# Kernel tuning notes

Measured on AMD Instinct MI355X. Metric: run time of the kernel, lower is better.

## Reference

```python
import jax, jax.numpy as jnp
import numpy as np

CLASSES = 21
IOU_THRESH = 0.5
ALPHA, GAMMA = 0.25, 2.0
CLS_W, REG_W = 1.0, 1.0


def _make_boxes(key, shape):
    # valid xyxy boxes: x1<x2, y1<y2 inside unit square
    k1, k2 = jax.random.split(key)
    xy1 = jax.random.uniform(k1, shape[:-1] + (2,)) * 0.8
    wh = jax.random.uniform(k2, shape[:-1] + (2,)) * 0.19 + 0.01
    return jnp.concatenate([xy1, xy1 + wh], axis=-1).astype(jnp.float32)


def setup_inputs() -> dict:
    key = jax.random.key(0)
    k1, k2, k3, k4, k5 = jax.random.split(key, 5)
    B, A, T = 4, 49152, 50
    return {
        "classification_preds": jax.random.normal(k1, (B, A, CLASSES), dtype=jnp.float32),
        "boxes_preds": _make_boxes(k2, (B, A, 4)),
        "anchors": _make_boxes(k3, (B, A, 4)),
        "target_boxes": _make_boxes(k4, (B, T, 4)),
        "target_labels": jax.random.randint(k5, (B, T), 1, CLASSES),  # 1..20 (0=background)
    }


def compute_iou(a, b):
    # a: [T,4] xyxy, b: [A,4] xyxy -> [T,A]
    lt = jnp.maximum(a[:, None, :2], b[None, :, :2])
    rb = jnp.minimum(a[:, None, 2:], b[None, :, 2:])
    wh = jnp.clip(rb - lt, 0.0)
    inter = wh[..., 0] * wh[..., 1]
    area_a = (a[:, 2] - a[:, 0]) * (a[:, 3] - a[:, 1])
    area_b = (b[:, 2] - b[:, 0]) * (b[:, 3] - b[:, 1])
    union = area_a[:, None] + area_b[None, :] - inter
    return inter / jnp.clip(union, 1e-8)


def encode(boxes, anchors):
    # xyxy -> center offsets relative to anchors
    bc = (boxes[:, :2] + boxes[:, 2:]) * 0.5
    bwh = boxes[:, 2:] - boxes[:, :2]
    ac = (anchors[:, :2] + anchors[:, 2:]) * 0.5
    awh = anchors[:, 2:] - anchors[:, :2]
    txy = (bc - ac) / awh
    twh = jnp.log(bwh / awh)
    return jnp.concatenate([txy, twh], axis=-1)


def focal_loss(logits, targets):
    p = jax.nn.sigmoid(logits)
    ce = -(targets * jax.nn.log_sigmoid(logits) + (1.0 - targets) * jax.nn.log_sigmoid(-logits))
    pt = targets * p + (1.0 - targets) * (1.0 - p)
    alpha_t = targets * ALPHA + (1.0 - targets) * (1.0 - ALPHA)
    return alpha_t * (1.0 - pt) ** GAMMA * ce


def smooth_l1(x, y):
    d = jnp.abs(x - y)
    return jnp.where(d < 1.0, 0.5 * d * d, d - 0.5)


def reference(classification_preds, boxes_preds, anchors, target_boxes, target_labels):
    cls = classification_preds.reshape(-1, CLASSES)   # [A, C]
    box = boxes_preds.reshape(-1, 4)                  # [A, 4]
    anc = anchors.reshape(-1, 4)                      # [A, 4]
    tb = target_boxes.reshape(-1, 4)                  # [T, 4]
    tl = target_labels.reshape(-1)                    # [T]

    iou = compute_iou(tb, anc)                        # [T, A]
    max_iou = jnp.max(iou, axis=0)                    # [A]
    tid = jnp.argmax(iou, axis=0)                     # [A]
    pos = max_iou >= IOU_THRESH                       # [A]
    pos_cnt = jnp.sum(pos.astype(jnp.int32))
    norm = jnp.clip(pos_cnt, 1).astype(cls.dtype)

    onehot = jax.nn.one_hot(tl[tid], CLASSES, dtype=cls.dtype)        # [A, C]
    background = jax.nn.one_hot(0, CLASSES, dtype=cls.dtype)          # [C]
    cls_tgt = jnp.where(pos[:, None], onehot, background[None, :])    # [A, C]

    cls_loss = jnp.sum(focal_loss(cls, cls_tgt)) / norm

    enc_pred = encode(box, anc)                       # [A, 4]
    enc_tgt = encode(tb[tid], anc)                    # [A, 4]
    reg_elem = smooth_l1(enc_pred, enc_tgt) * pos[:, None].astype(cls.dtype)
    reg_loss = jnp.sum(reg_elem) / (norm * 4.0)       # mean over positive elements
    reg_loss = jnp.where(pos_cnt > 0, reg_loss, 0.0)

    wc = cls_loss * CLS_W
    wr = reg_loss * REG_W
    return (wc + wr, wc, wr)
```

## Files before the change

kernel.cpp:

```cpp
#include <hip/hip_runtime.h>


#define CLASSES 21
#define TPB 256
#define G 4

__global__ void prep_kernel(const float4* __restrict__ tb,
                            float* __restrict__ tarea, int T) {
    int t = blockIdx.x * blockDim.x + threadIdx.x;
    if (t < T) {
        float4 v = tb[t];
        tarea[t] = (v.z - v.x) * (v.w - v.y);
    }
}

__global__ __launch_bounds__(TPB)
void iou_kernel(const float4* __restrict__ anc,
                const float4* __restrict__ tbox,
                const float* __restrict__ tarea,
                float* __restrict__ pbI, float* __restrict__ pbU,
                int* __restrict__ pbT,
                int A, int T, int chunk) {
    int c  = blockIdx.x & (G - 1);
    int ab = blockIdx.x >> 2;
    int a  = ab * TPB + threadIdx.x;
    if (a >= A) return;

    float4 av = anc[a];
    float areaA = (av.z - av.x) * (av.w - av.y);

    int t0 = c * chunk;
    int t1 = min(T, t0 + chunk);
    float bI = 0.0f, bU = 1.0f;
    int bT = t0;
    #pragma unroll 10
    for (int t = t0; t < t1; ++t) {
        float4 tv = tbox[t];
        float ta = tarea[t];
        float lx = fmaxf(tv.x, av.x);
        float ly = fmaxf(tv.y, av.y);
        float rx = fminf(tv.z, av.z);
        float ry = fminf(tv.w, av.w);
        float w = fmaxf(rx - lx, 0.0f);
        float h = fmaxf(ry - ly, 0.0f);
        float inter = w * h;
        float uni = (ta + areaA) - inter;
        bool gt = inter * bU > bI * uni;
        bI = gt ? inter : bI;
        bU = gt ? uni : bU;
        bT = gt ? t : bT;
    }
    size_t o = (size_t)c * A + a;
    pbI[o] = bI;
    pbU[o] = bU;
    pbT[o] = bT;
}

__global__ __launch_bounds__(TPB)
void loss_kernel(const float* __restrict__ cls,
                 const float4* __restrict__ box,
                 const float4* __restrict__ anc,
                 const int* __restrict__ labels,
                 const float4* __restrict__ tbox,
                 const float* __restrict__ pbI, const float* __restrict__ pbU,
                 const int* __restrict__ pbT,
                 float* __restrict__ pc, float* __restrict__ pr,
                 float* __restrict__ pp,
                 int A) {
    __shared__ float s_cls[TPB * CLASSES];
    int tid = threadIdx.x;
    int a = blockIdx.x * TPB + tid;

    {
        const float4* g4 = (const float4*)(cls + (size_t)blockIdx.x * TPB * CLASSES);
        float4* s4 = (float4*)s_cls;
        int n4 = (TPB * CLASSES) / 4;
        int lim4 = min(n4, (int)(((size_t)A * CLASSES - (size_t)blockIdx.x * TPB * CLASSES) / 4));
        for (int i = tid; i < lim4; i += TPB) s4[i] = g4[i];
    }
    __syncthreads();

    float cls_p = 0.0f, reg_p = 0.0f, pos_p = 0.0f;

    if (a < A) {
        float bI = 0.0f, bU = 1.0f;
        int bT = 0;
        #pragma unroll
        for (int c = 0; c < G; ++c) {
            size_t o = (size_t)c * A + a;
            float oI = pbI[o];
            float oU = pbU[o];
            int   oT = pbT[o];
            if (c == 0) { bI = oI; bU = oU; bT = oT; }
            else {
                bool gt = oI * bU > bI * oU;
                bI = gt ? oI : bI;
                bU = gt ? oU : bU;
                bT = gt ? oT : bT;
            }
        }
        bool pos = (bI + bI) >= bU;

        int hot = pos ? labels[bT] : 0;
        const float* crow = s_cls + tid * CLASSES;
        float csum = 0.0f;
        #pragma unroll
        for (int j = 0; j < CLASSES; ++j) {
            float x = crow[j];
            float y = (j == hot) ? -x : x;
            float em = __expf(-fabsf(y));
            float sp = fmaxf(y, 0.0f) + __logf(1.0f + em);
            float r1 = __builtin_amdgcn_rcpf(1.0f + em);
            float sg = (y >= 0.0f) ? r1 : em * r1;
            float f = sg * sg * sp;
            csum = fmaf(f, (j == hot) ? (1.0f / 3.0f) : 1.0f, csum);
        }
        cls_p = csum * 0.75f;

        if (pos) {
            pos_p = 1.0f;
            float4 av = anc[a];
            float4 bv = box[a];
            float4 tv = tbox[bT];
            float aw = av.z - av.x, ah = av.w - av.y;
            float acx = (av.x + av.z) * 0.5f, acy = (av.y + av.w) * 0.5f;
            float ep0 = ((bv.x + bv.z) * 0.5f - acx) / aw;
            float ep1 = ((bv.y + bv.w) * 0.5f - acy) / ah;
            float ep2 = __logf((bv.z - bv.x) / aw);
            float ep3 = __logf((bv.w - bv.y) / ah);
            float et0 = ((tv.x + tv.z) * 0.5f - acx) / aw;
            float et1 = ((tv.y + tv.w) * 0.5f - acy) / ah;
            float et2 = __logf((tv.z - tv.x) / aw);
            float et3 = __logf((tv.w - tv.y) / ah);
            float r = 0.0f, d;
            d = fabsf(ep0 - et0); r += (d < 1.0f) ? 0.5f * d * d : d - 0.5f;
            d = fabsf(ep1 - et1); r += (d < 1.0f) ? 0.5f * d * d : d - 0.5f;
            d = fabsf(ep2 - et2); r += (d < 1.0f) ? 0.5f * d * d : d - 0.5f;
            d = fabsf(ep3 - et3); r += (d < 1.0f) ? 0.5f * d * d : d - 0.5f;
            reg_p = r;
        }
    }

    #pragma unroll
    for (int off = 32; off > 0; off >>= 1) {
        cls_p += __shfl_down(cls_p, off, 64);
        reg_p += __shfl_down(reg_p, off, 64);
        pos_p += __shfl_down(pos_p, off, 64);
    }
    __shared__ float red[3][TPB / 64];
    int wave = tid >> 6;
    int lane = tid & 63;
    if (lane == 0) {
        red[0][wave] = cls_p;
        red[1][wave] = reg_p;
        red[2][wave] = pos_p;
    }
    __syncthreads();
    if (tid == 0) {
        float c = 0.0f, r = 0.0f, q = 0.0f;
        #pragma unroll
        for (int wv = 0; wv < TPB / 64; ++wv) {
            c += red[0][wv]; r += red[1][wv]; q += red[2][wv];
        }
        pc[blockIdx.x] = c;
        pr[blockIdx.x] = r;
        pp[blockIdx.x] = q;
    }
}

__global__ __launch_bounds__(TPB)
void fin_kernel(const float* __restrict__ pc,
                const float* __restrict__ pr,
                const float* __restrict__ pp,
                int nb, float* __restrict__ out) {
    int tid = threadIdx.x;
    float c = 0.0f, r = 0.0f, q = 0.0f;
    for (int i = tid; i < nb; i += TPB) {
        c += pc[i]; r += pr[i]; q += pp[i];
    }
    #pragma unroll
    for (int off = 32; off > 0; off >>= 1) {
        c += __shfl_down(c, off, 64);
        r += __shfl_down(r, off, 64);
        q += __shfl_down(q, off, 64);
    }
    __shared__ float red[3][TPB / 64];
    int wave = tid >> 6;
    int lane = tid & 63;
    if (lane == 0) { red[0][wave] = c; red[1][wave] = r; red[2][wave] = q; }
    __syncthreads();
    if (tid == 0) {
        float cs = 0.0f, rs = 0.0f, qs = 0.0f;
        #pragma unroll
        for (int wv = 0; wv < TPB / 64; ++wv) {
            cs += red[0][wv]; rs += red[1][wv]; qs += red[2][wv];
        }
        float norm = fmaxf(qs, 1.0f);
        float wc = cs / norm;
        float wr = (qs > 0.0f) ? rs / (norm * 4.0f) : 0.0f;
        out[0] = wc + wr;
        out[1] = wc;
        out[2] = wr;
    }
}

extern "C" void kernel_launch(void* const* d_in, const int* in_sizes, int n_in,
                              void* d_out, int out_size, void* d_ws, size_t ws_size,
                              hipStream_t stream) {
    const float* cls  = (const float*)d_in[0];
    const float4* box = (const float4*)d_in[1];
    const float4* anc = (const float4*)d_in[2];
    const float4* tb  = (const float4*)d_in[3];
    const int* tl     = (const int*)d_in[4];

    int A = in_sizes[0] / CLASSES;
    int T = in_sizes[4];
    int chunk = (T + G - 1) / G;

    float* tarea = (float*)d_ws;
    float* pbI   = (float*)((char*)d_ws + 4096);
    float* pbU   = pbI + (size_t)G * A;
    int*   pbT   = (int*)(pbU + (size_t)G * A);
    int nb2 = (A + TPB - 1) / TPB;
    float* pc = (float*)(pbT + (size_t)G * A);
    float* pr = pc + nb2;
    float* pp = pr + nb2;

    prep_kernel<<<(T + TPB - 1) / TPB, TPB, 0, stream>>>(tb, tarea, T);

    int nb1 = nb2 * G;
    iou_kernel<<<nb1, TPB, 0, stream>>>(anc, tb, tarea, pbI, pbU, pbT, A, T, chunk);

    loss_kernel<<<nb2, TPB, 0, stream>>>(cls, box, anc, tl, tb,
                                         pbI, pbU, pbT, pc, pr, pp, A);

    fin_kernel<<<1, TPB, 0, stream>>>(pc, pr, pp, nb2, (float*)d_out);
}
```

Measured before the change: 104.4 us.

## Drop prep and final kernels; fuse reduction via atomics and last-block finalize

Removes the target-area prep kernel by computing areas inline in the IoU loop, and has each IoU thread process two anchors so target box loads are amortized. The separate final reduction kernel is replaced by atomic accumulation with a last-block-done counter inside the loss kernel, with the accumulators reset by the first IoU block. This cuts two kernel launches at the cost of global atomics and a float summation order that is no longer deterministic.

Measured after the change: 139.1 us. 1.33x slower.

```diff
diff --git a/kernel.cpp b/kernel.cpp
--- a/kernel.cpp
+++ b/kernel.cpp
@@ -4,56 +4,75 @@
 #define CLASSES 21
 #define TPB 256
 #define G 4
-
-__global__ void prep_kernel(const float4* __restrict__ tb,
-                            float* __restrict__ tarea, int T) {
-    int t = blockIdx.x * blockDim.x + threadIdx.x;
-    if (t < T) {
-        float4 v = tb[t];
-        tarea[t] = (v.z - v.x) * (v.w - v.y);
-    }
-}
-
-__global__ __launch_bounds__(TPB)
+#define APT 2
+
+__global__ __launch_bounds__(TPB, 8)
 void iou_kernel(const float4* __restrict__ anc,
                 const float4* __restrict__ tbox,
-                const float* __restrict__ tarea,
                 float* __restrict__ pbI, float* __restrict__ pbU,
                 int* __restrict__ pbT,
+                float* __restrict__ accums, int* __restrict__ counter,
                 int A, int T, int chunk) {
+    if (blockIdx.x == 0) {
+        if (threadIdx.x < 3) atomicExch(&accums[threadIdx.x], 0.0f);
+        else if (threadIdx.x == 3) atomicExch(counter, 0);
+    }
+
     int c  = blockIdx.x & (G - 1);
     int ab = blockIdx.x >> 2;
-    int a  = ab * TPB + threadIdx.x;
-    if (a >= A) return;
-
-    float4 av = anc[a];
-    float areaA = (av.z - av.x) * (av.w - av.y);
+    int a0 = ab * (TPB * APT) + threadIdx.x;
+    int a1 = a0 + TPB;
+    if (a0 >= A) return;
+    bool has1 = (a1 < A);
+
+    float4 av0 = anc[a0];
+    float4 av1 = has1 ? anc[a1] : av0;
+    float areaA0 = (av0.z - av0.x) * (av0.w - av0.y);
+    float areaA1 = (av1.z - av1.x) * (av1.w - av1.y);
 
     int t0 = c * chunk;
     int t1 = min(T, t0 + chunk);
-    float bI = 0.0f, bU = 1.0f;
-    int bT = t0;
-    #pragma unroll 10
+    float bI0 = 0.0f, bU0 = 1.0f; int bT0 = t0;
+    float bI1 = 0.0f, bU1 = 1.0f; int bT1 = t0;
+    #pragma unroll 5
     for (int t = t0; t < t1; ++t) {
         float4 tv = tbox[t];
-        float ta = tarea[t];
-        float lx = fmaxf(tv.x, av.x);
-        float ly = fmaxf(tv.y, av.y);
-        float rx = fminf(tv.z, av.z);
-        float ry = fminf(tv.w, av.w);
-        float w = fmaxf(rx - lx, 0.0f);
-        float h = fmaxf(ry - ly, 0.0f);
-        float inter = w * h;
-        float uni = (ta + areaA) - inter;
-        bool gt = inter * bU > bI * uni;
-        bI = gt ? inter : bI;
-        bU = gt ? uni : bU;
-        bT = gt ? t : bT;
-    }
-    size_t o = (size_t)c * A + a;
-    pbI[o] = bI;
-    pbU[o] = bU;
-    pbT[o] = bT;
+        float ta = (tv.z - tv.x) * (tv.w - tv.y);
+        {
+            float lx = fmaxf(tv.x, av0.x);
+            float ly = fmaxf(tv.y, av0.y);
+            float rx = fminf(tv.z, av0.z);
+            float ry = fminf(tv.w, av0.w);
+            float w = fmaxf(rx - lx, 0.0f);
+            float h = fmaxf(ry - ly, 0.0f);
+            float inter = w * h;
+            float uni = (ta + areaA0) - inter;
+            bool gt = inter * bU0 > bI0 * uni;
+            bI0 = gt ? inter : bI0;
+            bU0 = gt ? uni : bU0;
+            bT0 = gt ? t : bT0;
+        }
+        {
+            float lx = fmaxf(tv.x, av1.x);
+            float ly = fmaxf(tv.y, av1.y);
+            float rx = fminf(tv.z, av1.z);
+            float ry = fminf(tv.w, av1.w);
+            float w = fmaxf(rx - lx, 0.0f);
+            float h = fmaxf(ry - ly, 0.0f);
+            float inter = w * h;
+            float uni = (ta + areaA1) - inter;
+            bool gt = inter * bU1 > bI1 * uni;
+            bI1 = gt ? inter : bI1;
+            bU1 = gt ? uni : bU1;
+            bT1 = gt ? t : bT1;
+        }
+    }
+    size_t o0 = (size_t)c * A + a0;
+    pbI[o0] = bI0; pbU[o0] = bU0; pbT[o0] = bT0;
+    if (has1) {
+        size_t o1 = o0 + TPB;
+        pbI[o1] = bI1; pbU[o1] = bU1; pbT[o1] = bT1;
+    }
 }
 
 __global__ __launch_bounds__(TPB)
@@ -64,8 +83,8 @@
                  const float4* __restrict__ tbox,
                  const float* __restrict__ pbI, const float* __restrict__ pbU,
                  const int* __restrict__ pbT,
-                 float* __restrict__ pc, float* __restrict__ pr,
-                 float* __restrict__ pp,
+                 float* __restrict__ accums, int* __restrict__ counter,
+                 float* __restrict__ out,
                  int A) {
     __shared__ float s_cls[TPB * CLASSES];
     int tid = threadIdx.x;
@@ -75,7 +94,8 @@
         const float4* g4 = (const float4*)(cls + (size_t)blockIdx.x * TPB * CLASSES);
         float4* s4 = (float4*)s_cls;
         int n4 = (TPB * CLASSES) / 4;
-        int lim4 = min(n4, (int)(((size_t)A * CLASSES - (size_t)blockIdx.x * TPB * CLASSES) / 4));
+        long long rem = ((long long)A * CLASSES - (long long)blockIdx.x * TPB * CLASSES) / 4;
+        int lim4 = (rem < n4) ? (int)rem : n4;
         for (int i = tid; i < lim4; i += TPB) s4[i] = g4[i];
     }
     __syncthreads();
@@ -156,45 +176,26 @@
         red[2][wave] = pos_p;
     }
     __syncthreads();
+
+    __shared__ int s_last;
     if (tid == 0) {
         float c = 0.0f, r = 0.0f, q = 0.0f;
         #pragma unroll
         for (int wv = 0; wv < TPB / 64; ++wv) {
             c += red[0][wv]; r += red[1][wv]; q += red[2][wv];
         }
-        pc[blockIdx.x] = c;
-        pr[blockIdx.x] = r;
-        pp[blockIdx.x] = q;
-    }
-}
-
-__global__ __launch_bounds__(TPB)
-void fin_kernel(const float* __restrict__ pc,
-                const float* __restrict__ pr,
-                const float* __restrict__ pp,
-                int nb, float* __restrict__ out) {
-    int tid = threadIdx.x;
-    float c = 0.0f, r = 0.0f, q = 0.0f;
-    for (int i = tid; i < nb; i += TPB) {
-        c += pc[i]; r += pr[i]; q += pp[i];
-    }
-    #pragma unroll
-    for (int off = 32; off > 0; off >>= 1) {
-        c += __shfl_down(c, off, 64);
-        r += __shfl_down(r, off, 64);
-        q += __shfl_down(q, off, 64);
-    }
-    __shared__ float red[3][TPB / 64];
-    int wave = tid >> 6;
-    int lane = tid & 63;
-    if (lane == 0) { red[0][wave] = c; red[1][wave] = r; red[2][wave] = q; }
+        atomicAdd(&accums[0], c);
+        atomicAdd(&accums[1], r);
+        atomicAdd(&accums[2], q);
+        __threadfence();
+        int old = atomicAdd(counter, 1);
+        s_last = (old == gridDim.x - 1) ? 1 : 0;
+    }
     __syncthreads();
-    if (tid == 0) {
-        float cs = 0.0f, rs = 0.0f, qs = 0.0f;
-        #pragma unroll
-        for (int wv = 0; wv < TPB / 64; ++wv) {
-            cs += red[0][wv]; rs += red[1][wv]; qs += red[2][wv];
-        }
+    if (s_last && tid == 0) {
+        float cs = atomicAdd(&accums[0], 0.0f);
+        float rs = atomicAdd(&accums[1], 0.0f);
+        float qs = atomicAdd(&accums[2], 0.0f);
         float norm = fmaxf(qs, 1.0f);
         float wc = cs / norm;
         float wr = (qs > 0.0f) ? rs / (norm * 4.0f) : 0.0f;
@@ -217,22 +218,18 @@
     int T = in_sizes[4];
     int chunk = (T + G - 1) / G;
 
-    float* tarea = (float*)d_ws;
-    float* pbI   = (float*)((char*)d_ws + 4096);
-    float* pbU   = pbI + (size_t)G * A;
-    int*   pbT   = (int*)(pbU + (size_t)G * A);
+    float* accums = (float*)d_ws;
+    int*   counter = (int*)(accums + 3);
+    float* pbI = (float*)((char*)d_ws + 4096);
+    float* pbU = pbI + (size_t)G * A;
+    int*   pbT = (int*)(pbU + (size_t)G * A);
+
+    int nb1 = ((A + TPB * APT - 1) / (TPB * APT)) * G;
+    iou_kernel<<<nb1, TPB, 0, stream>>>(anc, tb, pbI, pbU, pbT,
+                                        accums, counter, A, T, chunk);
+
     int nb2 = (A + TPB - 1) / TPB;
-    float* pc = (float*)(pbT + (size_t)G * A);
-    float* pr = pc + nb2;
-    float* pp = pr + nb2;
-
-    prep_kernel<<<(T + TPB - 1) / TPB, TPB, 0, stream>>>(tb, tarea, T);
-
-    int nb1 = nb2 * G;
-    iou_kernel<<<nb1, TPB, 0, stream>>>(anc, tb, tarea, pbI, pbU, pbT, A, T, chunk);
-
     loss_kernel<<<nb2, TPB, 0, stream>>>(cls, box, anc, tl, tb,
-                                         pbI, pbU, pbT, pc, pr, pp, A);
-
-    fin_kernel<<<1, TPB, 0, stream>>>(pc, pr, pp, nb2, (float*)d_out);
+                                         pbI, pbU, pbT,
+                                         accums, counter, (float*)d_out, A);
 }
```
